# Performance work log

Hardware: AMD Instinct MI355X
Metric: run time of the kernel (lower is better)

Reference implementation:

```python
import jax, jax.numpy as jnp
import numpy as np

# Module hyperparameters (init_kwargs)
L_ORDER = 10
R_ORDER = 2
L_STRIDE = 1
R_STRIDE = 1
D_V = 512

# Input dims
B, H, T = 16, 4, 1024


def setup_inputs() -> dict:
    key = jax.random.key(0)
    k1, k2, k3 = jax.random.split(key, 3)
    v = jax.random.normal(k1, (B, H, T, D_V), dtype=jnp.float32)
    # torch uses randn init; scale by 0.05 so the IIR recurrence over T=1024
    # frames stays numerically stable (same math, just a sane parameter point).
    l_filter = jax.random.normal(k2, (L_ORDER, D_V), dtype=jnp.float32) * 0.05
    r_filter = jax.random.normal(k3, (R_ORDER, D_V), dtype=jnp.float32) * 0.05
    return {"v": v, "l_filter": l_filter, "r_filter": r_filter}


def dfsmn_forward(v, l_filter, r_filter):
    # Semantics of the torch in-place loop over frames t = 0..T-1:
    #   p[t] = v[t] + l_filter[0]*v[t]                       (k=0 tap reads pre-update p[t]=v[t])
    #        + sum_{k=1}^{L-1} l_filter[k] * p[t - k*ls]     (past frames: ALREADY updated -> IIR)
    #        + sum_{j=1}^{R}   r_filter[j-1] * v[t + j*rs]   (future frames: NOT yet updated -> read v)
    # out-of-range taps are dropped (the while loops break).
    Bv, Hv, Tv, D = v.shape

    # "base" = everything that does not depend on updated past frames (fully vectorized)
    base = v * (1.0 + l_filter[0])  # (B,H,T,D)
    vpad = jnp.pad(v, ((0, 0), (0, 0), (0, R_ORDER * R_STRIDE), (0, 0)))
    for j in range(1, R_ORDER + 1):  # tiny fixed loop over right taps
        base = base + r_filter[j - 1] * jax.lax.dynamic_slice_in_dim(
            vpad, j * R_STRIDE, Tv, axis=2)

    # IIR part: p[t] = base[t] + sum_{k=1}^{L-1} l_filter[k] * p[t - k*ls]
    Wn = (L_ORDER - 1) * L_STRIDE  # history window length
    tap_idx = np.array([k * L_STRIDE - 1 for k in range(1, L_ORDER)])  # buf[i] = p[t-1-i]
    lf = l_filter[1:]  # (L-1, D)

    base_t = jnp.moveaxis(base, 2, 0)  # (T,B,H,D)
    buf0 = jnp.zeros((Wn, Bv, Hv, D), dtype=v.dtype)  # zeros == dropped out-of-range taps

    def step(buf, b_t):
        taps = buf[tap_idx]  # (L-1,B,H,D)
        p_t = b_t + jnp.einsum('kd,kbhd->bhd', lf, taps)
        buf = jnp.concatenate([p_t[None], buf[:-1]], axis=0)
        return buf, p_t

    _, p = jax.lax.scan(step, buf0, base_t)  # p: (T,B,H,D)
    return jnp.moveaxis(p, 0, 2)  # (B,H,T,D)


def reference(v, l_filter, r_filter):
    return dfsmn_forward(v, l_filter, r_filter)
```

## Files before the change

### kernel.cpp

```cpp
#include <hip/hip_runtime.h>

#define BB 16
#define HH 4
#define TT 1024
#define DD 512
#define NTAP 9
#define CHUNK 256
#define LOOKBACK 256


#define DFSMN_BLOCK(CUR, NXT, TB, STORE)                                     \
  {                                                                          \
    _Pragma("unroll")                                                        \
    for (int u = 0; u < 16; ++u) {                                           \
      const int idx = (TB) + 18 + u;                                         \
      NXT[u] = (idx < TT) ? vp[(size_t)idx * DD] : 0.0f;                     \
    }                                                                        \
    _Pragma("unroll")                                                        \
    for (int u = 0; u < 16; ++u) {                                           \
      const float vt  = (u == 0) ? w0 : ((u == 1) ? w1 : CUR[(u < 2) ? 0 : (u - 2)]); \
      const float vt1 = (u == 0) ? w1 : CUR[(u < 1) ? 0 : (u - 1)];          \
      const float vt2 = CUR[u];                                              \
      float p = fmaf(vt, c0, r0 * vt1);                                      \
      p = fmaf(r1, vt2, p);                                                  \
              \
      _Pragma("unroll")                                                      \
      for (int k = NTAP - 1; k >= 0; --k)                                    \
        p = fmaf(a[k], hist[(u + 15 - k) & 15], p);                          \
      hist[u & 15] = p;                                                      \
      if (STORE) __builtin_nontemporal_store(p, &op[(size_t)((TB) + u) * DD]); \
    }                                                                        \
    w0 = CUR[14];                                                            \
    w1 = CUR[15];                                                            \
  }

__global__ __launch_bounds__(256, 2) void dfsmn_kernel(
    const float* __restrict__ v,
    const float* __restrict__ lfilt,
    const float* __restrict__ rfilt,
    float* __restrict__ out)
{
    const int d  = blockIdx.x * 256 + threadIdx.x;
    const int bh = blockIdx.y;
    const int t_begin = blockIdx.z * CHUNK;
    const int t_end   = t_begin + CHUNK;
    const int ts = (t_begin >= LOOKBACK) ? (t_begin - LOOKBACK) : 0;

    const float* __restrict__ vp = v + (size_t)bh * TT * DD + d;
    float* __restrict__ op = out + (size_t)bh * TT * DD + d;

    const float c0 = 1.0f + lfilt[d];
    float a[NTAP];
#pragma unroll
    for (int k = 0; k < NTAP; ++k) a[k] = lfilt[(k + 1) * DD + d];
    const float r0 = rfilt[d];
    const float r1 = rfilt[DD + d];

    float hist[16];
#pragma unroll
    for (int i = 0; i < 16; ++i) hist[i] = 0.0f;

    float A0[16], A1[16];
    float w0 = vp[(size_t)ts * DD];
    float w1 = vp[(size_t)(ts + 1) * DD];
#pragma unroll
    for (int u = 0; u < 16; ++u) {
        const int idx = ts + 2 + u;
        A0[u] = (idx < TT) ? vp[(size_t)idx * DD] : 0.0f;
    }

    int tb = ts;
    for (; tb < t_begin; tb += 32) {
        DFSMN_BLOCK(A0, A1, tb, false)
        DFSMN_BLOCK(A1, A0, tb + 16, false)
    }
    for (; tb < t_end; tb += 32) {
        DFSMN_BLOCK(A0, A1, tb, true)
        DFSMN_BLOCK(A1, A0, tb + 16, true)
    }
}

extern "C" void kernel_launch(void* const* d_in, const int* in_sizes, int n_in,
                              void* d_out, int out_size, void* d_ws, size_t ws_size,
                              hipStream_t stream) {
    const float* v  = (const float*)d_in[0];
    const float* lf = (const float*)d_in[1];
    const float* rf = (const float*)d_in[2];
    float* out = (float*)d_out;

    dim3 grid(DD / 256, BB * HH, TT / CHUNK);
    dim3 block(256, 1, 1);
    dfsmn_kernel<<<grid, block, 0, stream>>>(v, lf, rf, out);
}
```

Baseline: 56.73 us.

## Process two channels per thread with float2 and halve time chunk

Each thread now handles two adjacent D channels through a float2 vector type, so loads and stores become 64-bit and the FMA chain may map to packed FMA instructions. To keep the same number of blocks, the time chunk shrinks from 256 to 128 while the lookback stays at 256. That makes the redundant warm-up recomputation relatively larger per stored frame, and it doubles register use for the history and staging arrays, which can reduce occupancy.

```diff
diff --git a/kernel.cpp b/kernel.cpp
--- a/kernel.cpp
+++ b/kernel.cpp
@@ -1,12 +1,19 @@
 #include <hip/hip_runtime.h>
+
+typedef float v2 __attribute__((ext_vector_type(2)));
 
 #define BB 16
 #define HH 4
 #define TT 1024
 #define DD 512
 #define NTAP 9
-#define CHUNK 256
+#define CHUNK 128
 #define LOOKBACK 256
+#define RS (DD / 2)
+
+static __device__ __forceinline__ v2 fma2(v2 a, v2 b, v2 c) {
+    v2 r; r[0] = fmaf(a[0], b[0], c[0]); r[1] = fmaf(a[1], b[1], c[1]); return r;
+}
 
 
 #define DFSMN_BLOCK(CUR, NXT, TB, STORE)                                     \
@@ -14,59 +21,61 @@
     _Pragma("unroll")                                                        \
     for (int u = 0; u < 16; ++u) {                                           \
       const int idx = (TB) + 18 + u;                                         \
-      NXT[u] = (idx < TT) ? vp[(size_t)idx * DD] : 0.0f;                     \
+      NXT[u] = (idx < TT) ? vp[(size_t)idx * RS] : (v2)0.0f;                 \
     }                                                                        \
     _Pragma("unroll")                                                        \
     for (int u = 0; u < 16; ++u) {                                           \
-      const float vt  = (u == 0) ? w0 : ((u == 1) ? w1 : CUR[(u < 2) ? 0 : (u - 2)]); \
-      const float vt1 = (u == 0) ? w1 : CUR[(u < 1) ? 0 : (u - 1)];          \
-      const float vt2 = CUR[u];                                              \
-      float p = fmaf(vt, c0, r0 * vt1);                                      \
-      p = fmaf(r1, vt2, p);                                                  \
-              \
+      const v2 vt  = (u == 0) ? w0 : ((u == 1) ? w1 : CUR[(u < 2) ? 0 : (u - 2)]); \
+      const v2 vt1 = (u == 0) ? w1 : CUR[(u < 1) ? 0 : (u - 1)];             \
+      const v2 vt2 = CUR[u];                                                 \
+      v2 p = fma2(vt, c0, r0 * vt1);                                         \
+      p = fma2(r1, vt2, p);                                                  \
+                 \
       _Pragma("unroll")                                                      \
       for (int k = NTAP - 1; k >= 0; --k)                                    \
-        p = fmaf(a[k], hist[(u + 15 - k) & 15], p);                          \
+        p = fma2(a[k], hist[(u + 15 - k) & 15], p);                          \
       hist[u & 15] = p;                                                      \
-      if (STORE) __builtin_nontemporal_store(p, &op[(size_t)((TB) + u) * DD]); \
+      if (STORE) __builtin_nontemporal_store(p, &op[(size_t)((TB) + u) * RS]); \
     }                                                                        \
     w0 = CUR[14];                                                            \
     w1 = CUR[15];                                                            \
   }
 
 __global__ __launch_bounds__(256, 2) void dfsmn_kernel(
-    const float* __restrict__ v,
+    const float* __restrict__ vf,
     const float* __restrict__ lfilt,
     const float* __restrict__ rfilt,
-    float* __restrict__ out)
+    float* __restrict__ outf)
 {
-    const int d  = blockIdx.x * 256 + threadIdx.x;
-    const int bh = blockIdx.y;
+    const int tid = threadIdx.x;
+    const int bh  = blockIdx.y;
     const int t_begin = blockIdx.z * CHUNK;
     const int t_end   = t_begin + CHUNK;
     const int ts = (t_begin >= LOOKBACK) ? (t_begin - LOOKBACK) : 0;
 
-    const float* __restrict__ vp = v + (size_t)bh * TT * DD + d;
-    float* __restrict__ op = out + (size_t)bh * TT * DD + d;
+    const v2* __restrict__ vp = (const v2*)(vf + (size_t)bh * TT * DD) + tid;
+    v2* __restrict__ op = (v2*)(outf + (size_t)bh * TT * DD) + tid;
 
-    const float c0 = 1.0f + lfilt[d];
-    float a[NTAP];
+    const v2* __restrict__ lf2 = (const v2*)lfilt;
+    const v2* __restrict__ rf2 = (const v2*)rfilt;
+    const v2 c0 = (v2)1.0f + lf2[tid];
+    v2 a[NTAP];
 #pragma unroll
-    for (int k = 0; k < NTAP; ++k) a[k] = lfilt[(k + 1) * DD + d];
-    const float r0 = rfilt[d];
-    const float r1 = rfilt[DD + d];
+    for (int k = 0; k < NTAP; ++k) a[k] = lf2[(size_t)(k + 1) * RS + tid];
+    const v2 r0 = rf2[tid];
+    const v2 r1 = rf2[RS + tid];
 
-    float hist[16];
+    v2 hist[16];
 #pragma unroll
-    for (int i = 0; i < 16; ++i) hist[i] = 0.0f;
+    for (int i = 0; i < 16; ++i) hist[i] = (v2)0.0f;
 
-    float A0[16], A1[16];
-    float w0 = vp[(size_t)ts * DD];
-    float w1 = vp[(size_t)(ts + 1) * DD];
+    v2 A0[16], A1[16];
+    v2 w0 = vp[(size_t)ts * RS];
+    v2 w1 = vp[(size_t)(ts + 1) * RS];
 #pragma unroll
     for (int u = 0; u < 16; ++u) {
         const int idx = ts + 2 + u;
-        A0[u] = (idx < TT) ? vp[(size_t)idx * DD] : 0.0f;
+        A0[u] = (idx < TT) ? vp[(size_t)idx * RS] : (v2)0.0f;
     }
 
     int tb = ts;
@@ -88,7 +97,7 @@
     const float* rf = (const float*)d_in[2];
     float* out = (float*)d_out;
 
-    dim3 grid(DD / 256, BB * HH, TT / CHUNK);
+    dim3 grid(1, BB * HH, TT / CHUNK);
     dim3 block(256, 1, 1);
     dfsmn_kernel<<<grid, block, 0, stream>>>(v, lf, rf, out);
 }
```

After: 67.69 us. 19.3% more time.
